# Optimization experiments

Hardware: AMD Instinct MI355X
Metric: run time of the kernel (lower is better)

The kernel has to match this reference:

```python
import jax, jax.numpy as jnp
import numpy as np

B, S, D, H, F = 2, 2048, 768, 12, 3072
DH = D // H  # head dim = 64


def setup_inputs() -> dict:
    key = jax.random.key(0)
    ks = jax.random.split(key, 16)
    sc = 0.02
    p = {
        "src": jax.random.normal(ks[0], (B, S, D), jnp.float32),
        # attention projections (torch Linear layout: [out, in], bias=True in xformers MultiHeadDispatch)
        "wq": jax.random.normal(ks[1], (D, D), jnp.float32) * sc,
        "bq": jnp.zeros((D,), jnp.float32),
        "wk": jax.random.normal(ks[2], (D, D), jnp.float32) * sc,
        "bk": jnp.zeros((D,), jnp.float32),
        "wv": jax.random.normal(ks[3], (D, D), jnp.float32) * sc,
        "bv": jnp.zeros((D,), jnp.float32),
        "wo": jax.random.normal(ks[4], (D, D), jnp.float32) * sc,
        "bo": jnp.zeros((D,), jnp.float32),
        # FFN: fc1 (bias) -> SwiGLU (two bias-free F->F projections) -> fc2 (bias)
        "w_fc1": jax.random.normal(ks[5], (F, D), jnp.float32) * sc,
        "b_fc1": jnp.zeros((F,), jnp.float32),
        "w_in": jax.random.normal(ks[6], (F, F), jnp.float32) * sc,
        "w_gate": jax.random.normal(ks[7], (F, F), jnp.float32) * sc,
        "w_fc2": jax.random.normal(ks[8], (D, F), jnp.float32) * sc,
        "b_fc2": jnp.zeros((D,), jnp.float32),
        # RMSNorm weights
        "g_attn": jnp.ones((D,), jnp.float32),
        "g_ffn": jnp.ones((D,), jnp.float32),
    }
    return p


def _rmsnorm(x, g):
    eps = jnp.asarray(jnp.finfo(x.dtype).eps, x.dtype)
    return x * jax.lax.rsqrt(jnp.mean(x * x, axis=-1, keepdims=True) + eps) * g


def _rope_cos_sin(seq_len, dim, dtype):
    # xformers RotaryEmbedding: inv_freq over even indices, emb = cat(freqs, freqs)
    inv_freq = 1.0 / (10000.0 ** (jnp.arange(0, dim, 2, dtype=jnp.float32) / dim))
    freqs = jnp.arange(seq_len, dtype=jnp.float32)[:, None] * inv_freq[None, :]  # [S, dim/2]
    emb = jnp.concatenate([freqs, freqs], axis=-1)  # [S, dim]
    return jnp.cos(emb).astype(dtype), jnp.sin(emb).astype(dtype)


def _rotate_half(x):
    x1, x2 = jnp.split(x, 2, axis=-1)
    return jnp.concatenate([-x2, x1], axis=-1)


def _apply_rope(x, cos, sin):
    # x: [B, H, S, DH]; cos/sin: [S, DH]
    return x * cos[None, None] + _rotate_half(x) * sin[None, None]


def _block(src, wq, bq, wk, bk, wv, bv, wo, bo,
           w_fc1, b_fc1, w_in, w_gate, w_fc2, b_fc2, g_attn, g_ffn):
    b, s, d = src.shape
    x = _rmsnorm(src, g_attn)
    q = (x @ wq.T + bq).reshape(b, s, H, DH).transpose(0, 2, 1, 3)
    k = (x @ wk.T + bk).reshape(b, s, H, DH).transpose(0, 2, 1, 3)
    v = (x @ wv.T + bv).reshape(b, s, H, DH).transpose(0, 2, 1, 3)
    cos, sin = _rope_cos_sin(s, DH, x.dtype)
    q = _apply_rope(q, cos, sin)
    k = _apply_rope(k, cos, sin)
    scale = 1.0 / np.sqrt(DH)
    scores = jnp.einsum("bhsd,bhtd->bhst", q * scale, k)  # non-causal, no mask
    attn = jax.nn.softmax(scores, axis=-1)
    ctx = jnp.einsum("bhst,bhtd->bhsd", attn, v)
    ctx = ctx.transpose(0, 2, 1, 3).reshape(b, s, d)
    attn_out = ctx @ wo.T + bo

    y = _rmsnorm(src + attn_out, g_ffn)
    h = y @ w_fc1.T + b_fc1
    h = (h @ w_in.T) * jax.nn.silu(h @ w_gate.T)  # SwiGLU
    ffn_out = h @ w_fc2.T + b_fc2
    return y + ffn_out


def reference(src, wq, bq, wk, bk, wv, bv, wo, bo,
              w_fc1, b_fc1, w_in, w_gate, w_fc2, b_fc2, g_attn, g_ffn):
    return _block(src, wq, bq, wk, bk, wv, bv, wo, bo,
                  w_fc1, b_fc1, w_in, w_gate, w_fc2, b_fc2, g_attn, g_ffn)
```

## Files before the change

kernel.cpp:

```cpp
#include <hip/hip_runtime.h>

#define DEV static __device__ __forceinline__

typedef __attribute__((ext_vector_type(8))) short bf16x8;
typedef __attribute__((ext_vector_type(4))) short short4v;
typedef __attribute__((ext_vector_type(4))) float f32x4;

DEV f32x4 mfma16(bf16x8 a, bf16x8 b, f32x4 c){
  return __builtin_amdgcn_mfma_f32_16x16x32_bf16(a, b, c, 0, 0, 0);
}
DEV float bf2f(short s){ union{unsigned u; float f;} v; v.u=((unsigned)(unsigned short)s)<<16; return v.f; }
DEV short f2bf(float f){ union{float f; unsigned u;} v; v.f=f; unsigned r=v.u+0x7fffu+((v.u>>16)&1u); return (short)(r>>16); }
DEV void gload16(const void* g, void* l){
  __builtin_amdgcn_global_load_lds((const __attribute__((address_space(1))) void*)g,
                                   (__attribute__((address_space(3))) void*)l, 16, 0, 0);
}
DEV int cvtpk(float lo, float hi){
  int r; asm("v_cvt_pk_bf16_f32 %0, %1, %2" : "=v"(r) : "v"(lo), "v"(hi)); return r;
}

enum { EPI_BF16=0, EPI_RESID=2, EPI_QKV=4 };

__global__ void k_convert7(const float* __restrict__ p0, const float* __restrict__ p1,
                           const float* __restrict__ p2, const float* __restrict__ p3,
                           const float* __restrict__ p4, const float* __restrict__ p5,
                           const float* __restrict__ p6, short* __restrict__ dst){
  int v = blockIdx.x * 256 + threadIdx.x;
  const float* src; int rel;
  if      (v <  147456){ src=p0; rel=v; }
  else if (v <  294912){ src=p1; rel=v-147456; }
  else if (v <  442368){ src=p2; rel=v-294912; }
  else if (v <  589824){ src=p3; rel=v-442368; }
  else if (v < 2949120){ src=p4; rel=v-589824; }
  else if (v < 5308416){ src=p5; rel=v-2949120; }
  else                 { src=p6; rel=v-5308416; }
  float4 x = ((const float4*)src)[rel];
  short4v o; o.x=f2bf(x.x); o.y=f2bf(x.y); o.z=f2bf(x.z); o.w=f2bf(x.w);
  int dv = (v < 589824) ? v : (v + 589824);
  ((short4v*)dst)[dv] = o;
}

__global__ void k_convertT(const float* __restrict__ in, short* __restrict__ out){
  __shared__ float lt[32][33];
  const int t = threadIdx.x;
  const int f0 = blockIdx.x * 32;
  const int d0 = blockIdx.y * 32;
  int r = t >> 3, c4 = t & 7;
  float4 v = *(const float4*)(in + (size_t)(f0 + r)*768 + d0 + c4*4);
  lt[r][c4*4+0] = v.x; lt[r][c4*4+1] = v.y; lt[r][c4*4+2] = v.z; lt[r][c4*4+3] = v.w;
  __syncthreads();
  short4v o;
  o.x = f2bf(lt[c4*4+0][r]);
  o.y = f2bf(lt[c4*4+1][r]);
  o.z = f2bf(lt[c4*4+2][r]);
  o.w = f2bf(lt[c4*4+3][r]);
  *(short4v*)(out + (size_t)(d0 + r)*3072 + f0 + c4*4) = o;
}

__global__ void k_gemv(const short* __restrict__ W, const float* __restrict__ b,
                       float* __restrict__ out){
  int row = blockIdx.x*4 + (threadIdx.x>>6);
  int lane = threadIdx.x & 63;
  const short* wr = W + (size_t)row*3072 + lane*48;
  const float* bb = b + lane*48;
  float s = 0.f;
  #pragma unroll
  for (int i=0;i<6;i++){
    bf16x8 w = *(const bf16x8*)(wr + i*8);
    float4 b0 = *(const float4*)(bb + i*8);
    float4 b1 = *(const float4*)(bb + i*8 + 4);
    s += bf2f(w[0])*b0.x + bf2f(w[1])*b0.y + bf2f(w[2])*b0.z + bf2f(w[3])*b0.w
       + bf2f(w[4])*b1.x + bf2f(w[5])*b1.y + bf2f(w[6])*b1.z + bf2f(w[7])*b1.w;
  }
  #pragma unroll
  for (int d=32; d>0; d>>=1) s += __shfl_xor(s, d);
  if (lane == 0) out[row] = s;
}

__global__ void k_rmsnorm(const float* __restrict__ x, const float* __restrict__ g,
                          short* __restrict__ out){
  int row = blockIdx.x*4 + (threadIdx.x>>6);
  int lane = threadIdx.x & 63;
  const float* xr = x + (size_t)row*768;
  float4 v[3];
  float ss = 0.f;
  #pragma unroll
  for (int i=0;i<3;i++){
    v[i] = *(const float4*)(xr + i*256 + lane*4);
    ss += v[i].x*v[i].x + v[i].y*v[i].y + v[i].z*v[i].z + v[i].w*v[i].w;
  }
  #pragma unroll
  for (int d=32; d>0; d>>=1) ss += __shfl_xor(ss, d);
  float sc = rsqrtf(ss*(1.f/768.f) + 1.1920929e-7f);
  #pragma unroll
  for (int i=0;i<3;i++){
    int c0 = i*256 + lane*4;
    float4 gv = *(const float4*)(g + c0);
    short4v o;
    o.x = f2bf(v[i].x*sc*gv.x); o.y = f2bf(v[i].y*sc*gv.y);
    o.z = f2bf(v[i].z*sc*gv.z); o.w = f2bf(v[i].w*sc*gv.w);
    *(short4v*)(out + (size_t)row*768 + c0) = o;
  }
}

template<int EPI>
__launch_bounds__(256, 2)
__global__ void k_gemm(const short* __restrict__ Aptr, const short* __restrict__ Bptr,
                       void* __restrict__ Cout, const float* __restrict__ bias,
                       const void* __restrict__ aux, const float* __restrict__ bias2,
                       const float* __restrict__ bias3, const void* __restrict__ aux2,
                       int M, int N, int K){
  __shared__ short ldsA[128*32];
  __shared__ short ldsB[128*32];
  const int t = threadIdx.x;
  const int wave = t >> 6, lane = t & 63;
  const int l15 = lane & 15, l4 = lane >> 4;
  const int nwg = gridDim.x * gridDim.y;
  const int bid0 = blockIdx.y * gridDim.x + blockIdx.x;
  const int cpx = nwg >> 3;
  const int bid = (bid0 & 7) * cpx + (bid0 >> 3);
  const int bm = bid / gridDim.x, bn = bid % gridDim.x;
  const int wr = wave >> 1, wc = wave & 1;

  f32x4 acc[4][4] = {};

  const short* Ag = Aptr + (size_t)(bm*128 + wave*32 + (lane>>2))*K + (lane&3)*8;
  const short* Bg = Bptr + (size_t)(bn*128 + wave*32 + (lane>>2))*K + (lane&3)*8;
  short* lA = ldsA + wave*1024;
  short* lB = ldsB + wave*1024;

  for (int k0 = 0; k0 < K; k0 += 32){
    __syncthreads();
    gload16(Ag + k0,                lA);
    gload16(Ag + k0 + 16*(size_t)K, lA + 512);
    gload16(Bg + k0,                lB);
    gload16(Bg + k0 + 16*(size_t)K, lB + 512);
    __syncthreads();
    bf16x8 af[4], bfr[4];
    #pragma unroll
    for (int m=0;m<4;m++) af[m]  = *(const bf16x8*)(ldsA + (wr*64 + m*16 + l15)*32 + l4*8);
    #pragma unroll
    for (int n=0;n<4;n++) bfr[n] = *(const bf16x8*)(ldsB + (wc*64 + n*16 + l15)*32 + l4*8);
    #pragma unroll
    for (int m=0;m<4;m++)
      #pragma unroll
      for (int n=0;n<4;n++)
        acc[m][n] = mfma16(af[m], bfr[n], acc[m][n]);
  }

  const int row0 = bm*128 + wr*64;
  const int col0 = bn*128 + wc*64;

  if constexpr (EPI == EPI_BF16){
    short* C = (short*)Cout;
    #pragma unroll
    for (int m=0;m<4;m++)
      #pragma unroll
      for (int j=0;j<4;j++){
        size_t rb = (size_t)(row0 + m*16 + l4*4 + j)*N + col0 + l15;
        #pragma unroll
        for (int n=0;n<4;n++) C[rb + n*16] = f2bf(acc[m][n][j]);
      }
  } else if constexpr (EPI == EPI_RESID){
    float* C = (float*)Cout;
    const float* srcf = (const float*)aux;
    float bvv[4];
    #pragma unroll
    for (int n=0;n<4;n++) bvv[n] = bias[col0 + n*16 + l15];
    #pragma unroll
    for (int m=0;m<4;m++)
      #pragma unroll
      for (int j=0;j<4;j++){
        size_t rb = (size_t)(row0 + m*16 + l4*4 + j)*N + col0 + l15;
        #pragma unroll
        for (int n=0;n<4;n++) C[rb + n*16] = acc[m][n][j] + bvv[n] + srcf[rb + n*16];
      }
  } else if constexpr (EPI == EPI_QKV){
    const int proj = col0 / 768;
    const int c768 = col0 - proj*768;
    const int h = c768 >> 6;
    const float* bs = proj==0 ? bias : (proj==1 ? bias2 : bias3);
    float bvv[4];
    #pragma unroll
    for (int n=0;n<4;n++) bvv[n] = bs[c768 + n*16 + l15];
    if (proj == 2){
      short* Ov = (short*)const_cast<void*>(aux2);
      #pragma unroll
      for (int m=0;m<4;m++){
        #pragma unroll
        for (int j=0;j<4;j++){
          int row = row0 + m*16 + l4*4 + j;
          int b = row >> 11, s = row & 2047;
          size_t hb = (size_t)(b*12 + h)*64;
          #pragma unroll
          for (int n=0;n<4;n++)
            Ov[(hb + n*16 + l15)*2048 + s] = f2bf(acc[m][n][j] + bvv[n]);
        }
      }
    } else {
      short* O = proj==0 ? (short*)Cout : (short*)const_cast<void*>(aux);
      const float sc = proj==0 ? 0.18033688011112042f : 1.0f;
      const float RC = 0.41524101186092034f;
      float invf0 = exp2f(-(float)l15 * RC);
      float invf1 = exp2f(-(float)(16 + l15) * RC);
      #pragma unroll
      for (int m=0;m<4;m++){
        #pragma unroll
        for (int j=0;j<4;j++){
          int row = row0 + m*16 + l4*4 + j;
          int b = row >> 11, s = row & 2047;
          size_t obase = ((size_t)(b*12 + h)*2048 + (size_t)s)*64;
          float a0 = acc[m][0][j] + bvv[0];
          float a1 = acc[m][1][j] + bvv[1];
          float a2 = acc[m][2][j] + bvv[2];
          float a3 = acc[m][3][j] + bvv[3];
          float sn0, cs0, sn1, cs1;
          __sincosf((float)s * invf0, &sn0, &cs0);
          __sincosf((float)s * invf1, &sn1, &cs1);
          O[obase + l15]      = f2bf((a0*cs0 - a2*sn0)*sc);
          O[obase + 16 + l15] = f2bf((a1*cs1 - a3*sn1)*sc);
          O[obase + 32 + l15] = f2bf((a2*cs0 + a0*sn0)*sc);
          O[obase + 48 + l15] = f2bf((a3*cs1 + a1*sn1)*sc);
        }
      }
    }
  }
}

__launch_bounds__(256, 2)
__global__ void k_wpart(const short* __restrict__ Aptr, const short* __restrict__ Bptr,
                        float* __restrict__ P){
  __shared__ short ldsA[128*32];
  __shared__ short ldsB[128*32];
  const int t = threadIdx.x;
  const int wave = t >> 6, lane = t & 63;
  const int l15 = lane & 15, l4 = lane >> 4;
  const int koff = blockIdx.z * 1536;
  const int bid0 = blockIdx.y * 6 + blockIdx.x;
  const int bid = (bid0 & 7) * 36 + (bid0 >> 3);
  const int bm = bid / 6, bn = bid % 6;
  const int wr = wave >> 1, wc = wave & 1;

  f32x4 acc[4][4] = {};

  const short* Ag = Aptr + (size_t)(bm*128 + wave*32 + (lane>>2))*3072 + (lane&3)*8 + koff;
  const short* Bg = Bptr + (size_t)(bn*128 + wave*32 + (lane>>2))*3072 + (lane&3)*8 + koff;
  short* lA = ldsA + wave*1024;
  short* lB = ldsB + wave*1024;

  for (int k0 = 0; k0 < 1536; k0 += 32){
    __syncthreads();
    gload16(Ag + k0,           lA);
    gload16(Ag + k0 + 16*3072, lA + 512);
    gload16(Bg + k0,           lB);
    gload16(Bg + k0 + 16*3072, lB + 512);
    __syncthreads();
    bf16x8 af[4], bfr[4];
    #pragma unroll
    for (int m=0;m<4;m++) af[m]  = *(const bf16x8*)(ldsA + (wr*64 + m*16 + l15)*32 + l4*8);
    #pragma unroll
    for (int n=0;n<4;n++) bfr[n] = *(const bf16x8*)(ldsB + (wc*64 + n*16 + l15)*32 + l4*8);
    #pragma unroll
    for (int m=0;m<4;m++)
      #pragma unroll
      for (int n=0;n<4;n++)
        acc[m][n] = mfma16(af[m], bfr[n], acc[m][n]);
  }

  float* Pz = P + (size_t)blockIdx.z * 4718592;
  const int row0 = bm*128 + wr*64;
  const int col0 = bn*128 + wc*64;
  #pragma unroll
  for (int m=0;m<4;m++)
    #pragma unroll
    for (int j=0;j<4;j++){
      size_t rb = (size_t)(row0 + m*16 + l4*4 + j)*768 + col0 + l15;
      #pragma unroll
      for (int n=0;n<4;n++) Pz[rb + n*16] = acc[m][n][j];
    }
}

__global__ void k_wred(const float* __restrict__ P, short* __restrict__ comp){
  int i = blockIdx.x * 256 + threadIdx.x;
  float4 a = ((const float4*)P)[i];
  float4 b = ((const float4*)(P + 4718592))[i];
  short4v o;
  o.x = f2bf(a.x + b.x); o.y = f2bf(a.y + b.y);
  o.z = f2bf(a.z + b.z); o.w = f2bf(a.w + b.w);
  ((short4v*)comp)[i] = o;
}

__launch_bounds__(256, 2)
__global__ void k_part(const short* __restrict__ Aptr, const short* __restrict__ Bptr,
                       float* __restrict__ Pa, float* __restrict__ Pb){
  __shared__ short ldsA[128*32];
  __shared__ short ldsB[128*32];
  const int t = threadIdx.x;
  const int wave = t >> 6, lane = t & 63;
  const int l15 = lane & 15, l4 = lane >> 4;
  const int K = 3072;
  const int z = blockIdx.z;
  const int koff = z * 768;
  const int bid0 = blockIdx.y * 6 + blockIdx.x;
  const int bid = (bid0 & 7) * 24 + (bid0 >> 3);
  const int bm = bid / 6, bn = bid % 6;
  const int wr = wave >> 1, wc = wave & 1;

  f32x4 acc[4][4] = {};

  const short* Ag = Aptr + (size_t)(bm*128 + wave*32 + (lane>>2))*K + (lane&3)*8 + koff;
  const short* Bg = Bptr + (size_t)(bn*128 + wave*32 + (lane>>2))*K + (lane&3)*8 + koff;
  short* lA = ldsA + wave*1024;
  short* lB = ldsB + wave*1024;

  for (int k0 = 0; k0 < 768; k0 += 32){
    __syncthreads();
    gload16(Ag + k0,                lA);
    gload16(Ag + k0 + 16*(size_t)K, lA + 512);
    gload16(Bg + k0,                lB);
    gload16(Bg + k0 + 16*(size_t)K, lB + 512);
    __syncthreads();
    bf16x8 af[4], bfr[4];
    #pragma unroll
    for (int m=0;m<4;m++) af[m]  = *(const bf16x8*)(ldsA + (wr*64 + m*16 + l15)*32 + l4*8);
    #pragma unroll
    for (int n=0;n<4;n++) bfr[n] = *(const bf16x8*)(ldsB + (wc*64 + n*16 + l15)*32 + l4*8);
    #pragma unroll
    for (int m=0;m<4;m++)
      #pragma unroll
      for (int n=0;n<4;n++)
        acc[m][n] = mfma16(af[m], bfr[n], acc[m][n]);
  }

  float* P = (z < 2) ? (Pa + (size_t)z*3145728) : (Pb + (size_t)(z-2)*3145728);
  const int row0 = bm*128 + wr*64;
  const int col0 = bn*128 + wc*64;
  #pragma unroll
  for (int m=0;m<4;m++)
    #pragma unroll
    for (int j=0;j<4;j++){
      size_t rb = (size_t)(row0 + m*16 + l4*4 + j)*768 + col0 + l15;
      #pragma unroll
      for (int n=0;n<4;n++) P[rb + n*16] = acc[m][n][j];
    }
}

__global__ void k_fc2red(const float* __restrict__ Pa, const float* __restrict__ Pb,
                         const float* __restrict__ bias, const short* __restrict__ yv,
                         float* __restrict__ out){
  int i = blockIdx.x * 256 + threadIdx.x;
  float4 a = ((const float4*)Pa)[i];
  float4 b = ((const float4*)(Pa + 3145728))[i];
  float4 c = ((const float4*)Pb)[i];
  float4 d = ((const float4*)(Pb + 3145728))[i];
  float4 bv = *(const float4*)(bias + (i % 192)*4);
  short4v y = ((const short4v*)yv)[i];
  float4 o;
  o.x = a.x + b.x + c.x + d.x + bv.x + bf2f(y.x);
  o.y = a.y + b.y + c.y + d.y + bv.y + bf2f(y.y);
  o.z = a.z + b.z + c.z + d.z + bv.z + bf2f(y.z);
  o.w = a.w + b.w + c.w + d.w + bv.w + bf2f(y.w);
  ((float4*)out)[i] = o;
}

__launch_bounds__(256, 2)
__global__ void k_ffglu(const short* __restrict__ Aptr, const short* __restrict__ Wcomp,
                        const float* __restrict__ bvg, short* __restrict__ Cout){
  __shared__ short lds[3*12288];
  const int tid = threadIdx.x;
  const int wave = tid >> 6, lane = tid & 63;
  const int l15 = lane & 15, l4 = lane >> 4;
  const int wm = wave >> 1, wn = wave & 1;
  const int K = 768, N = 3072;
  const int nt = 24;

  const int lin = blockIdx.y * 48 + blockIdx.x;
  const int xcd = lin & 7, idx = lin >> 3;
  const int bm = ((xcd & 1) << 3) + idx / 12;
  const int bn = (xcd >> 1) * 12 + idx % 12;

  const int srcC = ((lane & 3) ^ ((lane >> 3) & 3)) * 8;

  const short* aSrc[4];
  int aDst[4];
  #pragma unroll
  for (int i=0;i<4;i++){
    int s = i*4 + wave;
    int row = s*16 + (lane>>2);
    aSrc[i] = Aptr + (size_t)(bm*256 + row)*K + srcC;
    aDst[i] = s*512;
  }
  const short* bSrc[2];
  int bDst[2];
  #pragma unroll
  for (int i=0;i<2;i++){
    int j = i*4 + wave;
    int pidx = (j>>1)*16 + (lane>>2);
    int grow = (j & 1) ? 3072 : 0;
    bSrc[i] = Wcomp + (size_t)(grow + bn*64 + pidx)*K + srcC;
    bDst[i] = 8192 + j*512;
  }

  int offA[8], offB[4];
  #pragma unroll
  for (int m=0;m<8;m++){
    int r = wm*128 + m*16 + l15;
    offA[m] = r*32 + ((l4 ^ ((l15>>1)&3))<<3);
  }
  #pragma unroll
  for (int nf=0;nf<4;nf++){
    int r = wn*64 + nf*16 + l15;
    offB[nf] = 8192 + r*32 + ((l4 ^ ((l15>>1)&3))<<3);
  }

  f32x4 accv[8][2] = {};
  f32x4 accg[8][2] = {};

  short *b0 = lds, *b1 = lds + 12288, *b2 = lds + 24576;

  #define GSTAGE_ALL(buf, t) do{ \
    gload16(aSrc[0] + (size_t)(t)*32, (buf) + aDst[0]); \
    gload16(aSrc[1] + (size_t)(t)*32, (buf) + aDst[1]); \
    gload16(aSrc[2] + (size_t)(t)*32, (buf) + aDst[2]); \
    gload16(aSrc[3] + (size_t)(t)*32, (buf) + aDst[3]); \
    gload16(bSrc[0] + (size_t)(t)*32, (buf) + bDst[0]); \
    gload16(bSrc[1] + (size_t)(t)*32, (buf) + bDst[1]); \
  }while(0)

  GSTAGE_ALL(b0, 0);
  GSTAGE_ALL(b1, 1);

  for (int t = 0; t < nt; ++t){
    if (t < nt-1){
      asm volatile("s_waitcnt vmcnt(6)" ::: "memory");
    } else {
      asm volatile("s_waitcnt vmcnt(0)" ::: "memory");
    }
    __builtin_amdgcn_sched_barrier(0);
    __builtin_amdgcn_s_barrier();
    __builtin_amdgcn_sched_barrier(0);

    if (t + 2 < nt) GSTAGE_ALL(b2, t+2);

    bf16x8 a0 = *(const bf16x8*)(b0 + offA[0]);
    bf16x8 a1 = *(const bf16x8*)(b0 + offA[1]);
    bf16x8 a2 = *(const bf16x8*)(b0 + offA[2]);
    bf16x8 a3 = *(const bf16x8*)(b0 + offA[3]);
    bf16x8 a4 = *(const bf16x8*)(b0 + offA[4]);
    bf16x8 a5 = *(const bf16x8*)(b0 + offA[5]);
    bf16x8 a6 = *(const bf16x8*)(b0 + offA[6]);
    bf16x8 a7 = *(const bf16x8*)(b0 + offA[7]);
    bf16x8 v0 = *(const bf16x8*)(b0 + offB[0]);
    bf16x8 g0 = *(const bf16x8*)(b0 + offB[1]);
    bf16x8 v1 = *(const bf16x8*)(b0 + offB[2]);
    bf16x8 g1 = *(const bf16x8*)(b0 + offB[3]);

    __builtin_amdgcn_s_setprio(1);
    accv[0][0] = mfma16(a0, v0, accv[0][0]);  accg[0][0] = mfma16(a0, g0, accg[0][0]);
    accv[1][0] = mfma16(a1, v0, accv[1][0]);  accg[1][0] = mfma16(a1, g0, accg[1][0]);
    accv[2][0] = mfma16(a2, v0, accv[2][0]);  accg[2][0] = mfma16(a2, g0, accg[2][0]);
    accv[3][0] = mfma16(a3, v0, accv[3][0]);  accg[3][0] = mfma16(a3, g0, accg[3][0]);
    accv[0][1] = mfma16(a0, v1, accv[0][1]);  accg[0][1] = mfma16(a0, g1, accg[0][1]);
    accv[1][1] = mfma16(a1, v1, accv[1][1]);  accg[1][1] = mfma16(a1, g1, accg[1][1]);
    accv[2][1] = mfma16(a2, v1, accv[2][1]);  accg[2][1] = mfma16(a2, g1, accg[2][1]);
    accv[3][1] = mfma16(a3, v1, accv[3][1]);  accg[3][1] = mfma16(a3, g1, accg[3][1]);
    accv[4][0] = mfma16(a4, v0, accv[4][0]);  accg[4][0] = mfma16(a4, g0, accg[4][0]);
    accv[5][0] = mfma16(a5, v0, accv[5][0]);  accg[5][0] = mfma16(a5, g0, accg[5][0]);
    accv[6][0] = mfma16(a6, v0, accv[6][0]);  accg[6][0] = mfma16(a6, g0, accg[6][0]);
    accv[7][0] = mfma16(a7, v0, accv[7][0]);  accg[7][0] = mfma16(a7, g0, accg[7][0]);
    accv[4][1] = mfma16(a4, v1, accv[4][1]);  accg[4][1] = mfma16(a4, g1, accg[4][1]);
    accv[5][1] = mfma16(a5, v1, accv[5][1]);  accg[5][1] = mfma16(a5, g1, accg[5][1]);
    accv[6][1] = mfma16(a6, v1, accv[6][1]);  accg[6][1] = mfma16(a6, g1, accg[6][1]);
    accv[7][1] = mfma16(a7, v1, accv[7][1]);  accg[7][1] = mfma16(a7, g1, accg[7][1]);
    __builtin_amdgcn_s_setprio(0);

    short* tmp = b0; b0 = b1; b1 = b2; b2 = tmp;
  }
  #undef GSTAGE_ALL

  const int row0 = bm*256 + wm*128;
  #pragma unroll
  for (int m=0;m<8;m++){
    #pragma unroll
    for (int j=0;j<4;j++){
      size_t rb = (size_t)(row0 + m*16 + l4*4 + j)*N + bn*64 + wn*32 + l15;
      #pragma unroll
      for (int p=0;p<2;p++){
        int c = bn*64 + wn*32 + p*16 + l15;
        float g = accg[m][p][j] + bvg[3072 + c];
        float v = accv[m][p][j] + bvg[c];
        Cout[rb + p*16] = f2bf(v * g / (1.f + __expf(-g)));
      }
    }
  }
}

__launch_bounds__(256, 5)
__global__ void k_attn(const short* __restrict__ Q, const short* __restrict__ Kb,
                       const short* __restrict__ Vb, short* __restrict__ ctx){
  __shared__ short Kt[2][4096];
  __shared__ short Vt[2][4096];
  const int t = threadIdx.x, wave = t>>6, lane = t&63;
  const int l15 = lane&15, l4 = lane>>4;
  const int qt = blockIdx.x, bh = blockIdx.y;
  const short* Qh  = Q  + (size_t)bh*2048*64;
  const short* Kh  = Kb + (size_t)bh*2048*64;
  const short* Vth = Vb + (size_t)bh*64*2048;

  const int r7  = lane>>3;
  const int swz = ((lane&7) ^ r7) << 3;
  const int rr0 = wave*8 + r7, rr1 = 32 + wave*8 + r7;
  const size_t kOff0 = (size_t)rr0*64   + swz, kOff1 = (size_t)rr1*64   + swz;
  const size_t vOff0 = (size_t)rr0*2048 + swz, vOff1 = (size_t)rr1*2048 + swz;

  bf16x8 qf[2];
  #pragma unroll
  for (int kf=0;kf<2;kf++)
    qf[kf] = *(const bf16x8*)(Qh + (size_t)(qt*64 + wave*16 + l15)*64 + kf*32 + l4*8);

  f32x4 cacc[4] = {};
  f32x4 lacc = {};
  union { int w[4]; bf16x8 v; } onesf;
  onesf.w[0] = onesf.w[1] = onesf.w[2] = onesf.w[3] = 0x3F803F80;

  #define STAGE(sel, kv0) do { \
    const short* ksp = Kh + (size_t)(kv0)*64; \
    const short* vsp = Vth + (kv0); \
    short* kd = &Kt[sel][wave*512]; \
    short* vd = &Vt[sel][wave*512]; \
    gload16(ksp + kOff0, kd); \
    gload16(ksp + kOff1, kd + 2048); \
    gload16(vsp + vOff0, vd); \
    gload16(vsp + vOff1, vd + 2048); \
  } while(0)

  STAGE(0, 0);

  for (int tt = 0; tt < 32; ++tt){
    const int cur = tt & 1;
    if (tt < 31){
      STAGE(cur^1, (tt+1)*64);
      asm volatile("s_waitcnt vmcnt(4)" ::: "memory");
    } else {
      asm volatile("s_waitcnt vmcnt(0)" ::: "memory");
    }
    __builtin_amdgcn_sched_barrier(0);
    __builtin_amdgcn_s_barrier();
    __builtin_amdgcn_sched_barrier(0);

    const short* KtC = &Kt[cur][0];
    const short* VtC = &Vt[cur][0];

    f32x4 sacc[4] = {};
    __builtin_amdgcn_s_setprio(1);
    #pragma unroll
    for (int kf=0;kf<2;kf++){
      #pragma unroll
      for (int mk=0;mk<4;mk++){
        int r = mk*16 + l15;
        bf16x8 kfr = *(const bf16x8*)(KtC + r*64 + (((kf*4+l4) ^ (l15&7))<<3));
        sacc[mk] = mfma16(kfr, qf[kf], sacc[mk]);
      }
    }
    __builtin_amdgcn_s_setprio(0);

    int pk01[4], pk23[4];
    #pragma unroll
    for (int mk=0;mk<4;mk++){
      float p0 = exp2f(sacc[mk][0]);
      float p1 = exp2f(sacc[mk][1]);
      float p2 = exp2f(sacc[mk][2]);
      float p3 = exp2f(sacc[mk][3]);
      pk01[mk] = cvtpk(p0, p1);
      pk23[mk] = cvtpk(p2, p3);
    }

    #pragma unroll
    for (int ks=0;ks<2;ks++){
      int srcA = l15 + ((l4&1)<<5);
      int srcB = srcA + 16;
      int hi = l4>>1;
      int w0a = __shfl(pk01[2*ks], srcA), w0b = __shfl(pk01[2*ks+1], srcA);
      int w1a = __shfl(pk23[2*ks], srcA), w1b = __shfl(pk23[2*ks+1], srcA);
      int w2a = __shfl(pk01[2*ks], srcB), w2b = __shfl(pk01[2*ks+1], srcB);
      int w3a = __shfl(pk23[2*ks], srcB), w3b = __shfl(pk23[2*ks+1], srcB);
      union { int w[4]; bf16x8 v; } pa;
      pa.w[0] = hi ? w0b : w0a;
      pa.w[1] = hi ? w1b : w1a;
      pa.w[2] = hi ? w2b : w2a;
      pa.w[3] = hi ? w3b : w3a;
      __builtin_amdgcn_s_setprio(1);
      #pragma unroll
      for (int nf=0;nf<4;nf++){
        int dh = nf*16 + l15;
        bf16x8 vf = *(const bf16x8*)(VtC + dh*64 + (((ks*4+l4) ^ (dh&7))<<3));
        cacc[nf] = mfma16(pa.v, vf, cacc[nf]);
      }
      lacc = mfma16(pa.v, onesf.v, lacc);
      __builtin_amdgcn_s_setprio(0);
    }

    __builtin_amdgcn_sched_barrier(0);
    __builtin_amdgcn_s_barrier();
  }
  #undef STAGE

  const int b = bh/12, h = bh%12;
  #pragma unroll
  for (int j=0;j<4;j++){
    float inv = 1.f / lacc[j];
    int s = qt*64 + wave*16 + l4*4 + j;
    size_t base = ((size_t)b*2048 + s)*768 + h*64;
    #pragma unroll
    for (int nf=0;nf<4;nf++)
      ctx[base + nf*16 + l15] = f2bf(cacc[nf][j] * inv);
  }
}

extern "C" void kernel_launch(void* const* d_in, const int* in_sizes, int n_in,
                              void* d_out, int out_size, void* d_ws, size_t ws_size,
                              hipStream_t stream){
  (void)in_sizes; (void)n_in; (void)out_size;
  const float* src   = (const float*)d_in[0];
  const float* wq    = (const float*)d_in[1];
  const float* bq    = (const float*)d_in[2];
  const float* wk    = (const float*)d_in[3];
  const float* bk    = (const float*)d_in[4];
  const float* wv    = (const float*)d_in[5];
  const float* bv    = (const float*)d_in[6];
  const float* wo    = (const float*)d_in[7];
  const float* bo    = (const float*)d_in[8];
  const float* wfc1  = (const float*)d_in[9];
  const float* bfc1  = (const float*)d_in[10];
  const float* win   = (const float*)d_in[11];
  const float* wgate = (const float*)d_in[12];
  const float* wfc2  = (const float*)d_in[13];
  const float* bfc2  = (const float*)d_in[14];
  const float* gattn = (const float*)d_in[15];
  const float* gffn  = (const float*)d_in[16];

  char* ws = (char*)d_ws;
  constexpr size_t SZ_W768  = 768ull*768*2;
  constexpr size_t SZ_WFC   = 3072ull*768*2;
  constexpr size_t SZ_WFF   = 3072ull*3072*2;
  constexpr size_t SZ_ACT   = 4096ull*768*2;
  constexpr size_t SZ_ACTF  = 4096ull*768*4;
  constexpr size_t SZ_H     = 4096ull*3072*2;
  constexpr size_t OFF_WQ    = 0;
  constexpr size_t OFF_WK    = OFF_WQ + SZ_W768;
  constexpr size_t OFF_WV    = OFF_WK + SZ_W768;
  constexpr size_t OFF_WO    = OFF_WV + SZ_W768;
  constexpr size_t OFF_WFC1  = OFF_WO + SZ_W768;
  constexpr size_t OFF_WIN   = OFF_WFC1 + SZ_WFC;
  constexpr size_t OFF_WGATE = OFF_WIN + SZ_WFF;
  constexpr size_t OFF_WFC2  = OFF_WGATE + SZ_WFF;
  constexpr size_t OFF_XN    = OFF_WFC2 + SZ_WFC;
  constexpr size_t OFF_Q     = OFF_XN + SZ_ACT;
  constexpr size_t OFF_K     = OFF_Q + SZ_ACT;
  constexpr size_t OFF_V     = OFF_K + SZ_ACT;
  constexpr size_t OFF_RES   = OFF_V + SZ_ACT;
  constexpr size_t OFF_HIN   = OFF_RES + SZ_ACTF;
  constexpr size_t OFF_H2    = OFF_HIN + SZ_H;
  constexpr size_t WS_NEED   = OFF_H2 + SZ_H;
  if (ws_size < WS_NEED) return;

  constexpr size_t OFF_COMP  = OFF_HIN;
  constexpr size_t OFF_T     = OFF_HIN + 6144ull*768*2;
  constexpr size_t OFF_BVG   = OFF_T + 768ull*3072*2;

  short* wq_b    = (short*)(ws+OFF_WQ);
  short* win_b   = (short*)(ws+OFF_WIN);
  short* wfc2_b  = (short*)(ws+OFF_WFC2);
  short* wo_b    = (short*)(ws+OFF_WO);
  short* xn      = (short*)(ws+OFF_XN);
  short* ctxb    = (short*)(ws+OFF_XN);
  short* qb      = (short*)(ws+OFF_Q);
  short* yb      = (short*)(ws+OFF_Q);
  short* kb2     = (short*)(ws+OFF_K);
  short* vb2     = (short*)(ws+OFF_V);
  float* resid   = (float*)(ws+OFF_RES);
  short* comp    = (short*)(ws+OFF_COMP);
  short* wfc1T   = (short*)(ws+OFF_T);
  float* bvg     = (float*)(ws+OFF_BVG);
  short* h2      = (short*)(ws+OFF_H2);
  float* Pw      = (float*)(ws+OFF_XN);
  float* partA   = (float*)(ws+OFF_HIN);
  float* partB   = (float*)(ws+OFF_K);

  k_convert7<<<23040, 256, 0, stream>>>(wq, wk, wv, wo, win, wgate, wfc2, wq_b);
  k_convertT<<<dim3(96,24), 256, 0, stream>>>(wfc1, wfc1T);

  k_wpart<<<dim3(6,48,2), 256, 0, stream>>>(win_b, wfc1T, Pw);
  k_wred<<<4608, 256, 0, stream>>>(Pw, comp);
  k_gemv<<<1536, 256, 0, stream>>>(win_b, bfc1, bvg);

  k_rmsnorm<<<1024, 256, 0, stream>>>(src, gattn, xn);

  k_gemm<EPI_QKV><<<dim3(18,32), 256, 0, stream>>>(xn, wq_b, qb, bq, kb2, bk, bv, vb2, 4096, 2304, 768);

  k_attn<<<dim3(32, 24), 256, 0, stream>>>(qb, kb2, vb2, ctxb);

  k_gemm<EPI_RESID><<<dim3(6,32), 256, 0, stream>>>(ctxb, wo_b, resid, bo, src, nullptr, nullptr, nullptr, 4096, 768, 768);
  k_rmsnorm<<<1024, 256, 0, stream>>>(resid, gffn, yb);

  k_ffglu<<<dim3(48,16), 256, 0, stream>>>(yb, comp, bvg, h2);

  k_part<<<dim3(6,32,4), 256, 0, stream>>>(h2, wfc2_b, partA, partB);
  k_fc2red<<<3072, 256, 0, stream>>>(partA, partB, bfc2, yb, (float*)d_out);
}
```

Baseline: 283.9 us.

## Split attention KV range across waves with per-wave LDS and cross-wave reduction

Restructures the attention kernel so each block handles 32 queries and each of the four waves processes a quarter of the KV sequence independently. Each wave stages into its own LDS region, so the block-wide barriers inside the loop go away. Each wave also reuses its K fragments across two 16-query groups. Partial outputs and row sums are merged through LDS at the end, and the grid is linearised with a remapping of blocks to heads. The cost is twice as many blocks, more LDS per block and lower occupancy (launch bounds 2), and the staging within a wave is not double-buffered across iterations.

Measured after the change: 290.3 us. 2.3% more time.

```diff
diff --git a/kernel.cpp b/kernel.cpp
--- a/kernel.cpp
+++ b/kernel.cpp
@@ -495,126 +495,143 @@
   }
 }
 
-__launch_bounds__(256, 5)
+__launch_bounds__(256, 2)
 __global__ void k_attn(const short* __restrict__ Q, const short* __restrict__ Kb,
                        const short* __restrict__ Vb, short* __restrict__ ctx){
-  __shared__ short Kt[2][4096];
-  __shared__ short Vt[2][4096];
+  __shared__ short lds[4*8192];
   const int t = threadIdx.x, wave = t>>6, lane = t&63;
   const int l15 = lane&15, l4 = lane>>4;
-  const int qt = blockIdx.x, bh = blockIdx.y;
+  const int lin = blockIdx.x;
+  const int qq = lin >> 3, r8 = lin & 7;
+  const int bh = r8*3 + (qq % 3);
+  const int qt = qq / 3;
   const short* Qh  = Q  + (size_t)bh*2048*64;
-  const short* Kh  = Kb + (size_t)bh*2048*64;
-  const short* Vth = Vb + (size_t)bh*64*2048;
+  const short* Kh  = Kb + (size_t)bh*2048*64 + (size_t)wave*512*64;
+  const short* Vth = Vb + (size_t)bh*64*2048 + wave*512;
 
   const int r7  = lane>>3;
   const int swz = ((lane&7) ^ r7) << 3;
-  const int rr0 = wave*8 + r7, rr1 = 32 + wave*8 + r7;
-  const size_t kOff0 = (size_t)rr0*64   + swz, kOff1 = (size_t)rr1*64   + swz;
-  const size_t vOff0 = (size_t)rr0*2048 + swz, vOff1 = (size_t)rr1*2048 + swz;
-
-  bf16x8 qf[2];
-  #pragma unroll
-  for (int kf=0;kf<2;kf++)
-    qf[kf] = *(const bf16x8*)(Qh + (size_t)(qt*64 + wave*16 + l15)*64 + kf*32 + l4*8);
-
-  f32x4 cacc[4] = {};
-  f32x4 lacc = {};
+  short* myK = lds + wave*8192;
+  short* myV = myK + 4096;
+
+  bf16x8 qf[2][2];
+  #pragma unroll
+  for (int qg=0;qg<2;qg++)
+    #pragma unroll
+    for (int kf=0;kf<2;kf++)
+      qf[qg][kf] = *(const bf16x8*)(Qh + (size_t)(qt*32 + qg*16 + l15)*64 + kf*32 + l4*8);
+
+  f32x4 cacc[2][4] = {};
+  f32x4 lacc[2] = {};
   union { int w[4]; bf16x8 v; } onesf;
   onesf.w[0] = onesf.w[1] = onesf.w[2] = onesf.w[3] = 0x3F803F80;
 
-  #define STAGE(sel, kv0) do { \
-    const short* ksp = Kh + (size_t)(kv0)*64; \
-    const short* vsp = Vth + (kv0); \
-    short* kd = &Kt[sel][wave*512]; \
-    short* vd = &Vt[sel][wave*512]; \
-    gload16(ksp + kOff0, kd); \
-    gload16(ksp + kOff1, kd + 2048); \
-    gload16(vsp + vOff0, vd); \
-    gload16(vsp + vOff1, vd + 2048); \
-  } while(0)
-
-  STAGE(0, 0);
-
-  for (int tt = 0; tt < 32; ++tt){
-    const int cur = tt & 1;
-    if (tt < 31){
-      STAGE(cur^1, (tt+1)*64);
-      asm volatile("s_waitcnt vmcnt(4)" ::: "memory");
-    } else {
-      asm volatile("s_waitcnt vmcnt(0)" ::: "memory");
-    }
+  for (int tt = 0; tt < 8; ++tt){
+    const short* ksp = Kh + (size_t)tt*64*64;
+    const short* vsp = Vth + tt*64;
+    #pragma unroll
+    for (int i=0;i<8;i++) gload16(ksp + (size_t)(i*8 + r7)*64 + swz,   myK + i*512);
+    #pragma unroll
+    for (int i=0;i<8;i++) gload16(vsp + (size_t)(i*8 + r7)*2048 + swz, myV + i*512);
+    asm volatile("s_waitcnt vmcnt(8)" ::: "memory");
     __builtin_amdgcn_sched_barrier(0);
-    __builtin_amdgcn_s_barrier();
-    __builtin_amdgcn_sched_barrier(0);
-
-    const short* KtC = &Kt[cur][0];
-    const short* VtC = &Vt[cur][0];
-
-    f32x4 sacc[4] = {};
-    __builtin_amdgcn_s_setprio(1);
-    #pragma unroll
-    for (int kf=0;kf<2;kf++){
+
+    bf16x8 kfr[8];
+    #pragma unroll
+    for (int kf=0;kf<2;kf++)
       #pragma unroll
       for (int mk=0;mk<4;mk++){
         int r = mk*16 + l15;
-        bf16x8 kfr = *(const bf16x8*)(KtC + r*64 + (((kf*4+l4) ^ (l15&7))<<3));
-        sacc[mk] = mfma16(kfr, qf[kf], sacc[mk]);
+        kfr[kf*4+mk] = *(const bf16x8*)(myK + r*64 + (((kf*4+l4) ^ (l15&7))<<3));
+      }
+
+    int pk01[2][4], pk23[2][4];
+    #pragma unroll
+    for (int qg=0;qg<2;qg++){
+      f32x4 sacc[4] = {};
+      __builtin_amdgcn_s_setprio(1);
+      #pragma unroll
+      for (int kf=0;kf<2;kf++)
+        #pragma unroll
+        for (int mk=0;mk<4;mk++)
+          sacc[mk] = mfma16(kfr[kf*4+mk], qf[qg][kf], sacc[mk]);
+      __builtin_amdgcn_s_setprio(0);
+      #pragma unroll
+      for (int mk=0;mk<4;mk++){
+        float p0 = exp2f(sacc[mk][0]);
+        float p1 = exp2f(sacc[mk][1]);
+        float p2 = exp2f(sacc[mk][2]);
+        float p3 = exp2f(sacc[mk][3]);
+        pk01[qg][mk] = cvtpk(p0, p1);
+        pk23[qg][mk] = cvtpk(p2, p3);
       }
     }
-    __builtin_amdgcn_s_setprio(0);
-
-    int pk01[4], pk23[4];
-    #pragma unroll
-    for (int mk=0;mk<4;mk++){
-      float p0 = exp2f(sacc[mk][0]);
-      float p1 = exp2f(sacc[mk][1]);
-      float p2 = exp2f(sacc[mk][2]);
-      float p3 = exp2f(sacc[mk][3]);
-      pk01[mk] = cvtpk(p0, p1);
-      pk23[mk] = cvtpk(p2, p3);
-    }
+
+    asm volatile("s_waitcnt vmcnt(0)" ::: "memory");
+    __builtin_amdgcn_sched_barrier(0);
 
     #pragma unroll
     for (int ks=0;ks<2;ks++){
-      int srcA = l15 + ((l4&1)<<5);
-      int srcB = srcA + 16;
-      int hi = l4>>1;
-      int w0a = __shfl(pk01[2*ks], srcA), w0b = __shfl(pk01[2*ks+1], srcA);
-      int w1a = __shfl(pk23[2*ks], srcA), w1b = __shfl(pk23[2*ks+1], srcA);
-      int w2a = __shfl(pk01[2*ks], srcB), w2b = __shfl(pk01[2*ks+1], srcB);
-      int w3a = __shfl(pk23[2*ks], srcB), w3b = __shfl(pk23[2*ks+1], srcB);
-      union { int w[4]; bf16x8 v; } pa;
-      pa.w[0] = hi ? w0b : w0a;
-      pa.w[1] = hi ? w1b : w1a;
-      pa.w[2] = hi ? w2b : w2a;
-      pa.w[3] = hi ? w3b : w3a;
-      __builtin_amdgcn_s_setprio(1);
+      bf16x8 vf[4];
       #pragma unroll
       for (int nf=0;nf<4;nf++){
         int dh = nf*16 + l15;
-        bf16x8 vf = *(const bf16x8*)(VtC + dh*64 + (((ks*4+l4) ^ (dh&7))<<3));
-        cacc[nf] = mfma16(pa.v, vf, cacc[nf]);
-      }
-      lacc = mfma16(pa.v, onesf.v, lacc);
-      __builtin_amdgcn_s_setprio(0);
+        vf[nf] = *(const bf16x8*)(myV + dh*64 + (((ks*4+l4) ^ (dh&7))<<3));
+      }
+      #pragma unroll
+      for (int qg=0;qg<2;qg++){
+        int srcA = l15 + ((l4&1)<<5);
+        int srcB = srcA + 16;
+        int hi = l4>>1;
+        int w0a = __shfl(pk01[qg][2*ks], srcA), w0b = __shfl(pk01[qg][2*ks+1], srcA);
+        int w1a = __shfl(pk23[qg][2*ks], srcA), w1b = __shfl(pk23[qg][2*ks+1], srcA);
+        int w2a = __shfl(pk01[qg][2*ks], srcB), w2b = __shfl(pk01[qg][2*ks+1], srcB);
+        int w3a = __shfl(pk23[qg][2*ks], srcB), w3b = __shfl(pk23[qg][2*ks+1], srcB);
+        union { int w[4]; bf16x8 v; } pa;
+        pa.w[0] = hi ? w0b : w0a;
+        pa.w[1] = hi ? w1b : w1a;
+        pa.w[2] = hi ? w2b : w2a;
+        pa.w[3] = hi ? w3b : w3a;
+        __builtin_amdgcn_s_setprio(1);
+        #pragma unroll
+        for (int nf=0;nf<4;nf++)
+          cacc[qg][nf] = mfma16(pa.v, vf[nf], cacc[qg][nf]);
+        lacc[qg] = mfma16(pa.v, onesf.v, lacc[qg]);
+        __builtin_amdgcn_s_setprio(0);
+      }
     }
 
+    asm volatile("s_waitcnt lgkmcnt(0)" ::: "memory");
     __builtin_amdgcn_sched_barrier(0);
-    __builtin_amdgcn_s_barrier();
-  }
-  #undef STAGE
-
+  }
+
+  __syncthreads();
+  float* fb = (float*)lds;
+  float* lb = fb + 4*32*64;
+  #pragma unroll
+  for (int qg=0;qg<2;qg++){
+    #pragma unroll
+    for (int j=0;j<4;j++){
+      int q = qg*16 + l4*4 + j;
+      #pragma unroll
+      for (int nf=0;nf<4;nf++)
+        fb[(wave*32 + q)*64 + nf*16 + l15] = cacc[qg][nf][j];
+      if (l15 == 0) lb[wave*32 + q] = lacc[qg][j];
+    }
+  }
+  __syncthreads();
+  const int q = t >> 3, dh0 = (t & 7) * 8;
+  float linv = 1.f / (lb[q] + lb[32+q] + lb[64+q] + lb[96+q]);
   const int b = bh/12, h = bh%12;
-  #pragma unroll
-  for (int j=0;j<4;j++){
-    float inv = 1.f / lacc[j];
-    int s = qt*64 + wave*16 + l4*4 + j;
-    size_t base = ((size_t)b*2048 + s)*768 + h*64;
-    #pragma unroll
-    for (int nf=0;nf<4;nf++)
-      ctx[base + nf*16 + l15] = f2bf(cacc[nf][j] * inv);
-  }
+  short ov[8];
+  #pragma unroll
+  for (int i=0;i<8;i++){
+    int dh = dh0 + i;
+    float s = fb[q*64+dh] + fb[2048+q*64+dh] + fb[4096+q*64+dh] + fb[6144+q*64+dh];
+    ov[i] = f2bf(s * linv);
+  }
+  size_t base = ((size_t)b*2048 + qt*32 + q)*768 + h*64 + dh0;
+  *(bf16x8*)(ctx + base) = *(const bf16x8*)ov;
 }
 
 extern "C" void kernel_launch(void* const* d_in, const int* in_sizes, int n_in,
@@ -698,7 +715,7 @@
 
   k_gemm<EPI_QKV><<<dim3(18,32), 256, 0, stream>>>(xn, wq_b, qb, bq, kb2, bk, bv, vb2, 4096, 2304, 768);
 
-  k_attn<<<dim3(32, 24), 256, 0, stream>>>(qb, kb2, vb2, ctxb);
+  k_attn<<<1536, 256, 0, stream>>>(qb, kb2, vb2, ctxb);
 
   k_gemm<EPI_RESID><<<dim3(6,32), 256, 0, stream>>>(ctxb, wo_b, resid, bo, src, nullptr, nullptr, nullptr, 4096, 768, 768);
   k_rmsnorm<<<1024, 256, 0, stream>>>(resid, gffn, yb);
```
